# Performance work log

Measured on AMD Instinct MI355X. Metric: run time of the kernel, lower is better.

Reference implementation:

```python
import math
import jax, jax.numpy as jnp
import numpy as np

R = 15  # static Gaussian truncation radius (covers 3*sigma for resolutions up to ~12)
SIG_PER_FWHM = 1.0 / math.sqrt(8.0 * math.log(2.0))  # sigma = fwhm / sqrt(8 ln 2)


def _blur_resample_axis0(img, sigma, res):
    """Gaussian blur (dct2/symmetric boundary) + down/up resize along axis 0.

    img: [H, W]; sigma, res: scalars. anchor='f' resize convention:
      down (factor=1/res): low coord j samples input at j*res
      up   (factor=res, shape=H): out coord i samples low grid at i/res
    Low-res grid has n_low = max(floor(H/res), 1) valid rows; positions are
    clamped to the valid range (edge boundary).
    """
    H, W = img.shape
    dt = img.dtype
    # --- separable 1D Gaussian blur along axis 0 ---
    off = jnp.arange(-R, R + 1, dtype=dt)
    sig = jnp.maximum(sigma, jnp.asarray(1e-6, dt))
    w = jnp.exp(-0.5 * (off / sig) ** 2)
    w = w / w.sum()
    pad = jnp.pad(img, ((R, R), (0, 0)), mode='symmetric')  # dct2 boundary
    s = w[0] * pad[0:H]
    for k in range(1, 2 * R + 1):
        s = s + w[k] * pad[k:k + H]
    # --- downsample (factor = 1/res, anchor 'f') ---
    Hf = jnp.asarray(H, dt)
    n_low = jnp.maximum(jnp.floor(Hf / res), 1.0).astype(jnp.int32)
    pos = jnp.clip(jnp.arange(H, dtype=dt) * res, 0.0, Hf - 1.0)
    lo = jnp.floor(pos)
    fr = (pos - lo)[:, None]
    lo_i = lo.astype(jnp.int32)
    hi_i = jnp.minimum(lo_i + 1, H - 1)
    low = s[lo_i] * (1.0 - fr) + s[hi_i] * fr  # [H, W], rows >= n_low unused
    # --- upsample back to H (factor = res, anchor 'f') ---
    pos2 = jnp.clip(jnp.arange(H, dtype=dt) / res, 0.0, n_low.astype(dt) - 1.0)
    lo2 = jnp.floor(pos2)
    fr2 = (pos2 - lo2)[:, None]
    lo2_i = jnp.minimum(lo2.astype(jnp.int32), n_low - 1)
    hi2_i = jnp.minimum(lo2_i + 1, n_low - 1)
    return low[lo2_i] * (1.0 - fr2) + low[hi2_i] * fr2


def _process_one(img, res, ax, gp):
    fwhm = res * gp
    sigma = fwhm * SIG_PER_FWHM
    out0 = _blur_resample_axis0(img, sigma, res)          # degrade axis 0 (H)
    out1 = _blur_resample_axis0(img.T, sigma, res).T      # degrade axis 1 (W)
    return jnp.where(ax == 0, out0, out1)


def setup_inputs() -> dict:
    key = jax.random.key(0)
    k_x, k_res, k_ax, k_gap = jax.random.split(key, 4)
    B, C, H, W = 16, 4, 512, 512
    x = jax.random.normal(k_x, (B, C, H, W), dtype=jnp.float32)
    # lognormal with mean 3, sd 3 -> underlying normal params
    m, sdev = 3.0, 3.0
    var_log = math.log(1.0 + (sdev / m) ** 2)
    mu = math.log(m) - 0.5 * var_log
    z = jax.random.normal(k_res, (B, C), dtype=jnp.float32)
    resolution = jnp.clip(jnp.exp(mu + math.sqrt(var_log) * z), 1.0, None)
    axis = jax.random.randint(k_ax, (B, C), 0, 2, dtype=jnp.int32)
    gap = jax.random.uniform(k_gap, (B, C), dtype=jnp.float32)
    return {"x": x, "resolution": resolution, "axis": axis, "gap": gap}


def reference(x, resolution, axis, gap):
    B, C, H, W = x.shape
    flat = x.reshape(B * C, H, W)
    out = jax.vmap(_process_one)(flat, resolution.reshape(-1), axis.reshape(-1), gap.reshape(-1))
    return out.reshape(B, C, H, W)
```

## Files before the change

### kernel.cpp

```cpp
#include <hip/hip_runtime.h>
#include <math.h>


#define RR 15
#define TAPS 31
#define SIG_PER_FWHM 0.42466090014400953f
#define SWB(b) ((b) ^ (((b) >> 3) & 7))

typedef float f4v __attribute__((ext_vector_type(4)));
typedef float f2v __attribute__((ext_vector_type(2)));

__global__ __launch_bounds__(256) void lowres2d_kernel(
    const float* __restrict__ x,
    const float* __restrict__ resolution,
    const int*   __restrict__ axis,
    const float* __restrict__ gap,
    float* __restrict__ out)
{
    const int tid = threadIdx.x;
    const int n   = blockIdx.y;
    const int bx  = blockIdx.x;

    const float res = resolution[n];
    const int   ax  = axis[n];
    const float gp  = gap[n];

    const float sig = fmaxf(res * gp * SIG_PER_FWHM, 1e-6f);
    int n_low = (int)floorf(512.0f / res);
    if (n_low < 1) n_low = 1;
    if (n_low > 512) n_low = 512;
    const float nlm1f = (float)(n_low - 1);

    int kr = (int)(sig * 5.2565f) + 1;
    if (kr > RR) kr = RR;
    const int k0 = RR - kr, k1 = RR + 1 + kr;
    const int la_lo = kr, la_hi = 510 - kr;

    __shared__ float2 wd[32];
    __shared__ __align__(16) float smem[8192];
    float (*s_imgT)[4]   = (float (*)[4])smem;
    float (*s_lowT)[4]   = (float (*)[4])(smem + 4096);
    float (*s_lowB)[512] = (float (*)[512])smem;

    if (tid < 32) {
        const int k = tid;
        float r = 0.0f;
        if (k < TAPS) {
            float d = (float)(k - RR) / sig;
            r = expf(-0.5f * d * d);
        }
        float tot = r;
        tot += __shfl_xor(tot, 1, 32);
        tot += __shfl_xor(tot, 2, 32);
        tot += __shfl_xor(tot, 4, 32);
        tot += __shfl_xor(tot, 8, 32);
        tot += __shfl_xor(tot, 16, 32);
        float rm1 = __shfl_up(r, 1, 32);
        if (k == 0) rm1 = 0.0f;
        const float inv = 1.0f / tot;
        wd[k] = make_float2(r * inv, (rm1 - r) * inv);
    }
    __syncthreads();

    const size_t base = (size_t)n * (512 * 512);
    const float* img = x + base;
    float* o = out + base;

    if (ax == 0) {
        const int i0 = bx * 8;
        const int g  = tid >> 7;
        const int lt = tid & 127;
        const float4* img4 = (const float4*)img;

        float pA = fminf((float)i0 / res, nlm1f);
        int jlo = (int)floorf(pA);
        float pB = fminf((float)(i0 + 7) / res, nlm1f);
        int jhi = (int)floorf(pB) + 1;
        if (jhi > n_low - 1) jhi = n_low - 1;
        if (jhi < jlo) jhi = jlo;
        const int nrows = jhi - jlo + 1;

        for (int p = 0; p < nrows; p += 2) {
            int rowoff = p + g;
            int j = jlo + ((rowoff < nrows) ? rowoff : (nrows - 1));
            float pos = fminf((float)j * res, 511.0f);
            float lof = floorf(pos);
            float fr  = pos - lof;
            int   la  = __builtin_amdgcn_readfirstlane((int)lof);
            float4 acc = make_float4(0.0f, 0.0f, 0.0f, 0.0f);
            if (la >= la_lo && la <= la_hi) {
                #pragma unroll 4
                for (int k = k0; k <= k1; ++k) {
                    int t = la - RR + k;
                    float2 w = wd[k];
                    float cw = fmaf(fr, w.y, w.x);
                    float4 v = img4[(size_t)(t * 128 + lt)];
                    acc.x = fmaf(cw, v.x, acc.x);
                    acc.y = fmaf(cw, v.y, acc.y);
                    acc.z = fmaf(cw, v.z, acc.z);
                    acc.w = fmaf(cw, v.w, acc.w);
                }
            } else {
                for (int k = k0; k <= k1; ++k) {
                    int t = la - RR + k;
                    t = (t < 0)   ? (-1 - t)   : t;
                    t = (t > 511) ? (1023 - t) : t;
                    float2 w = wd[k];
                    float cw = fmaf(fr, w.y, w.x);
                    float4 v = img4[(size_t)(t * 128 + lt)];
                    acc.x = fmaf(cw, v.x, acc.x);
                    acc.y = fmaf(cw, v.y, acc.y);
                    acc.z = fmaf(cw, v.z, acc.z);
                    acc.w = fmaf(cw, v.w, acc.w);
                }
            }
            if (rowoff < nrows) {
                ((float4*)&s_lowB[rowoff][0])[lt] = acc;
            }
        }
        __syncthreads();

        #pragma unroll
        for (int p = 0; p < 4; ++p) {
            int i = i0 + p * 2 + g;
            float pos2 = fminf((float)i / res, nlm1f);
            float l2f  = floorf(pos2);
            float fr2  = pos2 - l2f;
            int lo2 = (int)l2f;
            int hi2 = (lo2 + 1 <= jhi) ? (lo2 + 1) : jhi;
            float4 A = ((float4*)&s_lowB[lo2 - jlo][0])[lt];
            float4 B = ((float4*)&s_lowB[hi2 - jlo][0])[lt];
            float omf2 = 1.0f - fr2;
            f4v ov = { A.x * omf2 + B.x * fr2,
                       A.y * omf2 + B.y * fr2,
                       A.z * omf2 + B.z * fr2,
                       A.w * omf2 + B.w * fr2 };
            __builtin_nontemporal_store(ov, (f4v*)o + (size_t)(i * 128 + lt));
        }
    } else {
        const int h0 = bx * 8;
        const float* imgr = img + (size_t)h0 * 512;

        #pragma unroll
        for (int p = 0; p < 2; ++p) {
            int c = p * 256 + tid;
            float v0 = imgr[0 * 512 + c];
            float v1 = imgr[1 * 512 + c];
            float v2 = imgr[2 * 512 + c];
            float v3 = imgr[3 * 512 + c];
            float v4 = imgr[4 * 512 + c];
            float v5 = imgr[5 * 512 + c];
            float v6 = imgr[6 * 512 + c];
            float v7 = imgr[7 * 512 + c];
            *(float4*)&s_imgT[SWB(2 * c + 0)][0] = make_float4(v0, v1, v2, v3);
            *(float4*)&s_imgT[SWB(2 * c + 1)][0] = make_float4(v4, v5, v6, v7);
        }
        __syncthreads();

        for (int j = tid; j < n_low; j += 256) {
            float pos = fminf((float)j * res, 511.0f);
            float lof = floorf(pos);
            float fr  = pos - lof;
            int   la  = (int)lof;
            float a0 = 0.f, a1 = 0.f, a2 = 0.f, a3 = 0.f;
            float a4 = 0.f, a5 = 0.f, a6 = 0.f, a7 = 0.f;
            if (la >= la_lo && la <= la_hi) {
                #pragma unroll 4
                for (int k = k0; k <= k1; ++k) {
                    int t = la - RR + k;
                    float2 w = wd[k];
                    float cw = fmaf(fr, w.y, w.x);
                    float4 u = *(const float4*)&s_imgT[SWB(2 * t + 0)][0];
                    float4 v = *(const float4*)&s_imgT[SWB(2 * t + 1)][0];
                    a0 = fmaf(cw, u.x, a0);
                    a1 = fmaf(cw, u.y, a1);
                    a2 = fmaf(cw, u.z, a2);
                    a3 = fmaf(cw, u.w, a3);
                    a4 = fmaf(cw, v.x, a4);
                    a5 = fmaf(cw, v.y, a5);
                    a6 = fmaf(cw, v.z, a6);
                    a7 = fmaf(cw, v.w, a7);
                }
            } else {
                for (int k = k0; k <= k1; ++k) {
                    int t = la - RR + k;
                    t = (t < 0)   ? (-1 - t)   : t;
                    t = (t > 511) ? (1023 - t) : t;
                    float2 w = wd[k];
                    float cw = fmaf(fr, w.y, w.x);
                    float4 u = *(const float4*)&s_imgT[SWB(2 * t + 0)][0];
                    float4 v = *(const float4*)&s_imgT[SWB(2 * t + 1)][0];
                    a0 = fmaf(cw, u.x, a0);
                    a1 = fmaf(cw, u.y, a1);
                    a2 = fmaf(cw, u.z, a2);
                    a3 = fmaf(cw, u.w, a3);
                    a4 = fmaf(cw, v.x, a4);
                    a5 = fmaf(cw, v.y, a5);
                    a6 = fmaf(cw, v.z, a6);
                    a7 = fmaf(cw, v.w, a7);
                }
            }
            *(float4*)&s_lowT[SWB(2 * j + 0)][0] = make_float4(a0, a1, a2, a3);
            *(float4*)&s_lowT[SWB(2 * j + 1)][0] = make_float4(a4, a5, a6, a7);
        }
        __syncthreads();

        {
            int ia = 2 * tid, ib = 2 * tid + 1;
            float posa = fminf((float)ia / res, nlm1f);
            float posb = fminf((float)ib / res, nlm1f);
            float lfa = floorf(posa), lfb = floorf(posb);
            float fra = posa - lfa,   frb = posb - lfb;
            int loa = (int)lfa, lob = (int)lfb;
            int hia = (loa + 1 < n_low) ? (loa + 1) : (n_low - 1);
            int hib = (lob + 1 < n_low) ? (lob + 1) : (n_low - 1);
            float oma = 1.0f - fra, omb = 1.0f - frb;
            float4 Aa0 = *(const float4*)&s_lowT[SWB(2 * loa + 0)][0];
            float4 Aa1 = *(const float4*)&s_lowT[SWB(2 * loa + 1)][0];
            float4 Ba0 = *(const float4*)&s_lowT[SWB(2 * hia + 0)][0];
            float4 Ba1 = *(const float4*)&s_lowT[SWB(2 * hia + 1)][0];
            float4 Ab0 = *(const float4*)&s_lowT[SWB(2 * lob + 0)][0];
            float4 Ab1 = *(const float4*)&s_lowT[SWB(2 * lob + 1)][0];
            float4 Bb0 = *(const float4*)&s_lowT[SWB(2 * hib + 0)][0];
            float4 Bb1 = *(const float4*)&s_lowT[SWB(2 * hib + 1)][0];
            float Aar[8] = {Aa0.x, Aa0.y, Aa0.z, Aa0.w, Aa1.x, Aa1.y, Aa1.z, Aa1.w};
            float Bar[8] = {Ba0.x, Ba0.y, Ba0.z, Ba0.w, Ba1.x, Ba1.y, Ba1.z, Ba1.w};
            float Abr[8] = {Ab0.x, Ab0.y, Ab0.z, Ab0.w, Ab1.x, Ab1.y, Ab1.z, Ab1.w};
            float Bbr[8] = {Bb0.x, Bb0.y, Bb0.z, Bb0.w, Bb1.x, Bb1.y, Bb1.z, Bb1.w};
            #pragma unroll
            for (int r = 0; r < 8; ++r) {
                float va = Aar[r] * oma + Bar[r] * fra;
                float vb = Abr[r] * omb + Bbr[r] * frb;
                f2v ov = { va, vb };
                __builtin_nontemporal_store(
                    ov, (f2v*)(o + (size_t)(h0 + r) * 512) + tid);
            }
        }
    }
}

extern "C" void kernel_launch(void* const* d_in, const int* in_sizes, int n_in,
                              void* d_out, int out_size, void* d_ws, size_t ws_size,
                              hipStream_t stream) {
    const float* x          = (const float*)d_in[0];
    const float* resolution = (const float*)d_in[1];
    const int*   axis       = (const int*)d_in[2];
    const float* gap        = (const float*)d_in[3];
    float* out = (float*)d_out;

    const int n_img = in_sizes[1];

    dim3 grid(64, n_img);
    lowres2d_kernel<<<grid, 256, 0, stream>>>(x, resolution, axis, gap, out);
}
```

Before: 119.4 us.

## Process two 8-row segments per block and prefetch the second tile

Each block now handles 16 rows (two 8-row segments) and the grid is halved. This amortizes per-block setup such as the weight computation. On the axis-1 path, the second 8-row tile is loaded into registers before the first tile's low-res computation, so global load latency overlaps with compute. Global loads also change to float2 per thread. The trade-off is fewer blocks for occupancy and extra registers and barriers.

```diff
diff --git a/kernel.cpp b/kernel.cpp
--- a/kernel.cpp
+++ b/kernel.cpp
@@ -67,145 +67,134 @@
     float* o = out + base;
 
     if (ax == 0) {
-        const int i0 = bx * 8;
+        const float4* img4 = (const float4*)img;
         const int g  = tid >> 7;
         const int lt = tid & 127;
-        const float4* img4 = (const float4*)img;
-
-        float pA = fminf((float)i0 / res, nlm1f);
-        int jlo = (int)floorf(pA);
-        float pB = fminf((float)(i0 + 7) / res, nlm1f);
-        int jhi = (int)floorf(pB) + 1;
-        if (jhi > n_low - 1) jhi = n_low - 1;
-        if (jhi < jlo) jhi = jlo;
-        const int nrows = jhi - jlo + 1;
-
-        for (int p = 0; p < nrows; p += 2) {
-            int rowoff = p + g;
-            int j = jlo + ((rowoff < nrows) ? rowoff : (nrows - 1));
-            float pos = fminf((float)j * res, 511.0f);
-            float lof = floorf(pos);
-            float fr  = pos - lof;
-            int   la  = __builtin_amdgcn_readfirstlane((int)lof);
-            float4 acc = make_float4(0.0f, 0.0f, 0.0f, 0.0f);
-            if (la >= la_lo && la <= la_hi) {
-                #pragma unroll 4
-                for (int k = k0; k <= k1; ++k) {
-                    int t = la - RR + k;
-                    float2 w = wd[k];
-                    float cw = fmaf(fr, w.y, w.x);
-                    float4 v = img4[(size_t)(t * 128 + lt)];
-                    acc.x = fmaf(cw, v.x, acc.x);
-                    acc.y = fmaf(cw, v.y, acc.y);
-                    acc.z = fmaf(cw, v.z, acc.z);
-                    acc.w = fmaf(cw, v.w, acc.w);
+
+        for (int seg = 0; seg < 2; ++seg) {
+            const int i0 = bx * 16 + seg * 8;
+
+            float pA = fminf((float)i0 / res, nlm1f);
+            int jlo = (int)floorf(pA);
+            float pB = fminf((float)(i0 + 7) / res, nlm1f);
+            int jhi = (int)floorf(pB) + 1;
+            if (jhi > n_low - 1) jhi = n_low - 1;
+            if (jhi < jlo) jhi = jlo;
+            const int nrows = jhi - jlo + 1;
+
+            for (int p = 0; p < nrows; p += 2) {
+                int rowoff = p + g;
+                int j = jlo + ((rowoff < nrows) ? rowoff : (nrows - 1));
+                float pos = fminf((float)j * res, 511.0f);
+                float lof = floorf(pos);
+                float fr  = pos - lof;
+                int   la  = __builtin_amdgcn_readfirstlane((int)lof);
+                float4 acc = make_float4(0.0f, 0.0f, 0.0f, 0.0f);
+                if (la >= la_lo && la <= la_hi) {
+                    #pragma unroll 4
+                    for (int k = k0; k <= k1; ++k) {
+                        int t = la - RR + k;
+                        float2 w = wd[k];
+                        float cw = fmaf(fr, w.y, w.x);
+                        float4 v = img4[(size_t)(t * 128 + lt)];
+                        acc.x = fmaf(cw, v.x, acc.x);
+                        acc.y = fmaf(cw, v.y, acc.y);
+                        acc.z = fmaf(cw, v.z, acc.z);
+                        acc.w = fmaf(cw, v.w, acc.w);
+                    }
+                } else {
+                    for (int k = k0; k <= k1; ++k) {
+                        int t = la - RR + k;
+                        t = (t < 0)   ? (-1 - t)   : t;
+                        t = (t > 511) ? (1023 - t) : t;
+                        float2 w = wd[k];
+                        float cw = fmaf(fr, w.y, w.x);
+                        float4 v = img4[(size_t)(t * 128 + lt)];
+                        acc.x = fmaf(cw, v.x, acc.x);
+                        acc.y = fmaf(cw, v.y, acc.y);
+                        acc.z = fmaf(cw, v.z, acc.z);
+                        acc.w = fmaf(cw, v.w, acc.w);
+                    }
                 }
-            } else {
-                for (int k = k0; k <= k1; ++k) {
-                    int t = la - RR + k;
-                    t = (t < 0)   ? (-1 - t)   : t;
-                    t = (t > 511) ? (1023 - t) : t;
-                    float2 w = wd[k];
-                    float cw = fmaf(fr, w.y, w.x);
-                    float4 v = img4[(size_t)(t * 128 + lt)];
-                    acc.x = fmaf(cw, v.x, acc.x);
-                    acc.y = fmaf(cw, v.y, acc.y);
-                    acc.z = fmaf(cw, v.z, acc.z);
-                    acc.w = fmaf(cw, v.w, acc.w);
+                if (rowoff < nrows) {
+                    ((float4*)&s_lowB[rowoff][0])[lt] = acc;
                 }
             }
-            if (rowoff < nrows) {
-                ((float4*)&s_lowB[rowoff][0])[lt] = acc;
-            }
-        }
-        __syncthreads();
-
-        #pragma unroll
-        for (int p = 0; p < 4; ++p) {
-            int i = i0 + p * 2 + g;
-            float pos2 = fminf((float)i / res, nlm1f);
-            float l2f  = floorf(pos2);
-            float fr2  = pos2 - l2f;
-            int lo2 = (int)l2f;
-            int hi2 = (lo2 + 1 <= jhi) ? (lo2 + 1) : jhi;
-            float4 A = ((float4*)&s_lowB[lo2 - jlo][0])[lt];
-            float4 B = ((float4*)&s_lowB[hi2 - jlo][0])[lt];
-            float omf2 = 1.0f - fr2;
-            f4v ov = { A.x * omf2 + B.x * fr2,
-                       A.y * omf2 + B.y * fr2,
-                       A.z * omf2 + B.z * fr2,
-                       A.w * omf2 + B.w * fr2 };
-            __builtin_nontemporal_store(ov, (f4v*)o + (size_t)(i * 128 + lt));
+            __syncthreads();
+
+            #pragma unroll
+            for (int p = 0; p < 4; ++p) {
+                int i = i0 + p * 2 + g;
+                float pos2 = fminf((float)i / res, nlm1f);
+                float l2f  = floorf(pos2);
+                float fr2  = pos2 - l2f;
+                int lo2 = (int)l2f;
+                int hi2 = (lo2 + 1 <= jhi) ? (lo2 + 1) : jhi;
+                float4 A = ((float4*)&s_lowB[lo2 - jlo][0])[lt];
+                float4 B = ((float4*)&s_lowB[hi2 - jlo][0])[lt];
+                float omf2 = 1.0f - fr2;
+                f4v ov = { A.x * omf2 + B.x * fr2,
+                           A.y * omf2 + B.y * fr2,
+                           A.z * omf2 + B.z * fr2,
+                           A.w * omf2 + B.w * fr2 };
+                __builtin_nontemporal_store(ov, (f4v*)o + (size_t)(i * 128 + lt));
+            }
+            if (seg == 0) __syncthreads();
         }
     } else {
-        const int h0 = bx * 8;
+        const int h0 = bx * 16;
         const float* imgr = img + (size_t)h0 * 512;
 
-        #pragma unroll
-        for (int p = 0; p < 2; ++p) {
-            int c = p * 256 + tid;
-            float v0 = imgr[0 * 512 + c];
-            float v1 = imgr[1 * 512 + c];
-            float v2 = imgr[2 * 512 + c];
-            float v3 = imgr[3 * 512 + c];
-            float v4 = imgr[4 * 512 + c];
-            float v5 = imgr[5 * 512 + c];
-            float v6 = imgr[6 * 512 + c];
-            float v7 = imgr[7 * 512 + c];
-            *(float4*)&s_imgT[SWB(2 * c + 0)][0] = make_float4(v0, v1, v2, v3);
-            *(float4*)&s_imgT[SWB(2 * c + 1)][0] = make_float4(v4, v5, v6, v7);
-        }
-        __syncthreads();
-
-        for (int j = tid; j < n_low; j += 256) {
-            float pos = fminf((float)j * res, 511.0f);
-            float lof = floorf(pos);
-            float fr  = pos - lof;
-            int   la  = (int)lof;
-            float a0 = 0.f, a1 = 0.f, a2 = 0.f, a3 = 0.f;
-            float a4 = 0.f, a5 = 0.f, a6 = 0.f, a7 = 0.f;
-            if (la >= la_lo && la <= la_hi) {
-                #pragma unroll 4
-                for (int k = k0; k <= k1; ++k) {
-                    int t = la - RR + k;
-                    float2 w = wd[k];
-                    float cw = fmaf(fr, w.y, w.x);
-                    float4 u = *(const float4*)&s_imgT[SWB(2 * t + 0)][0];
-                    float4 v = *(const float4*)&s_imgT[SWB(2 * t + 1)][0];
-                    a0 = fmaf(cw, u.x, a0);
-                    a1 = fmaf(cw, u.y, a1);
-                    a2 = fmaf(cw, u.z, a2);
-                    a3 = fmaf(cw, u.w, a3);
-                    a4 = fmaf(cw, v.x, a4);
-                    a5 = fmaf(cw, v.y, a5);
-                    a6 = fmaf(cw, v.z, a6);
-                    a7 = fmaf(cw, v.w, a7);
+        auto low_phase = [&]() {
+            for (int j = tid; j < n_low; j += 256) {
+                float pos = fminf((float)j * res, 511.0f);
+                float lof = floorf(pos);
+                float fr  = pos - lof;
+                int   la  = (int)lof;
+                float a0 = 0.f, a1 = 0.f, a2 = 0.f, a3 = 0.f;
+                float a4 = 0.f, a5 = 0.f, a6 = 0.f, a7 = 0.f;
+                if (la >= la_lo && la <= la_hi) {
+                    #pragma unroll 4
+                    for (int k = k0; k <= k1; ++k) {
+                        int t = la - RR + k;
+                        float2 w = wd[k];
+                        float cw = fmaf(fr, w.y, w.x);
+                        float4 u = *(const float4*)&s_imgT[SWB(2 * t + 0)][0];
+                        float4 v = *(const float4*)&s_imgT[SWB(2 * t + 1)][0];
+                        a0 = fmaf(cw, u.x, a0);
+                        a1 = fmaf(cw, u.y, a1);
+                        a2 = fmaf(cw, u.z, a2);
+                        a3 = fmaf(cw, u.w, a3);
+                        a4 = fmaf(cw, v.x, a4);
+                        a5 = fmaf(cw, v.y, a5);
+                        a6 = fmaf(cw, v.z, a6);
+                        a7 = fmaf(cw, v.w, a7);
+                    }
+                } else {
+                    for (int k = k0; k <= k1; ++k) {
+                        int t = la - RR + k;
+                        t = (t < 0)   ? (-1 - t)   : t;
+                        t = (t > 511) ? (1023 - t) : t;
+                        float2 w = wd[k];
+                        float cw = fmaf(fr, w.y, w.x);
+                        float4 u = *(const float4*)&s_imgT[SWB(2 * t + 0)][0];
+                        float4 v = *(const float4*)&s_imgT[SWB(2 * t + 1)][0];
+                        a0 = fmaf(cw, u.x, a0);
+                        a1 = fmaf(cw, u.y, a1);
+                        a2 = fmaf(cw, u.z, a2);
+                        a3 = fmaf(cw, u.w, a3);
+                        a4 = fmaf(cw, v.x, a4);
+                        a5 = fmaf(cw, v.y, a5);
+                        a6 = fmaf(cw, v.z, a6);
+                        a7 = fmaf(cw, v.w, a7);
+                    }
                 }
-            } else {
-                for (int k = k0; k <= k1; ++k) {
-                    int t = la - RR + k;
-                    t = (t < 0)   ? (-1 - t)   : t;
-                    t = (t > 511) ? (1023 - t) : t;
-                    float2 w = wd[k];
-                    float cw = fmaf(fr, w.y, w.x);
-                    float4 u = *(const float4*)&s_imgT[SWB(2 * t + 0)][0];
-                    float4 v = *(const float4*)&s_imgT[SWB(2 * t + 1)][0];
-                    a0 = fmaf(cw, u.x, a0);
-                    a1 = fmaf(cw, u.y, a1);
-                    a2 = fmaf(cw, u.z, a2);
-                    a3 = fmaf(cw, u.w, a3);
-                    a4 = fmaf(cw, v.x, a4);
-                    a5 = fmaf(cw, v.y, a5);
-                    a6 = fmaf(cw, v.z, a6);
-                    a7 = fmaf(cw, v.w, a7);
-                }
-            }
-            *(float4*)&s_lowT[SWB(2 * j + 0)][0] = make_float4(a0, a1, a2, a3);
-            *(float4*)&s_lowT[SWB(2 * j + 1)][0] = make_float4(a4, a5, a6, a7);
-        }
-        __syncthreads();
-
-        {
+                *(float4*)&s_lowT[SWB(2 * j + 0)][0] = make_float4(a0, a1, a2, a3);
+                *(float4*)&s_lowT[SWB(2 * j + 1)][0] = make_float4(a4, a5, a6, a7);
+            }
+        };
+
+        auto upsample = [&](int hrow) {
             int ia = 2 * tid, ib = 2 * tid + 1;
             float posa = fminf((float)ia / res, nlm1f);
             float posb = fminf((float)ib / res, nlm1f);
@@ -233,9 +222,48 @@
                 float vb = Abr[r] * omb + Bbr[r] * frb;
                 f2v ov = { va, vb };
                 __builtin_nontemporal_store(
-                    ov, (f2v*)(o + (size_t)(h0 + r) * 512) + tid);
-            }
+                    ov, (f2v*)(o + (size_t)(hrow + r) * 512) + tid);
+            }
+        };
+
+        {
+            f2v va[8];
+            #pragma unroll
+            for (int r = 0; r < 8; ++r)
+                va[r] = *(const f2v*)(imgr + (size_t)r * 512 + 2 * tid);
+            *(float4*)&s_imgT[SWB(4 * tid + 0)][0] =
+                make_float4(va[0].x, va[1].x, va[2].x, va[3].x);
+            *(float4*)&s_imgT[SWB(4 * tid + 1)][0] =
+                make_float4(va[4].x, va[5].x, va[6].x, va[7].x);
+            *(float4*)&s_imgT[SWB(4 * tid + 2)][0] =
+                make_float4(va[0].y, va[1].y, va[2].y, va[3].y);
+            *(float4*)&s_imgT[SWB(4 * tid + 3)][0] =
+                make_float4(va[4].y, va[5].y, va[6].y, va[7].y);
         }
+        __syncthreads();
+
+        f2v vb[8];
+        #pragma unroll
+        for (int r = 0; r < 8; ++r)
+            vb[r] = *(const f2v*)(imgr + (size_t)(8 + r) * 512 + 2 * tid);
+
+        low_phase();
+        __syncthreads();
+
+        upsample(h0);
+        *(float4*)&s_imgT[SWB(4 * tid + 0)][0] =
+            make_float4(vb[0].x, vb[1].x, vb[2].x, vb[3].x);
+        *(float4*)&s_imgT[SWB(4 * tid + 1)][0] =
+            make_float4(vb[4].x, vb[5].x, vb[6].x, vb[7].x);
+        *(float4*)&s_imgT[SWB(4 * tid + 2)][0] =
+            make_float4(vb[0].y, vb[1].y, vb[2].y, vb[3].y);
+        *(float4*)&s_imgT[SWB(4 * tid + 3)][0] =
+            make_float4(vb[4].y, vb[5].y, vb[6].y, vb[7].y);
+        __syncthreads();
+
+        low_phase();
+        __syncthreads();
+        upsample(h0 + 8);
     }
 }
 
@@ -250,6 +278,6 @@
 
     const int n_img = in_sizes[1];
 
-    dim3 grid(64, n_img);
+    dim3 grid(32, n_img);
     lowres2d_kernel<<<grid, 256, 0, stream>>>(x, resolution, axis, gap, out);
 }
```

Result: slower. 125.1 us (+4.8%).
